# Performance work log

Measured on AMD Instinct MI355X. Metric: run time of the kernel, lower is better.

Reference implementation:

```python
import jax, jax.numpy as jnp
import numpy as np

B, S, D = 4, 2048, 1024
E, TOP_K = 8, 2
N_FF = 4096
H = int(2 * N_FF / 3)  # 2730, Expert hidden when ffn_multiplier is None


def setup_inputs() -> dict:
    key = jax.random.key(0)
    ks = jax.random.split(key, 8)
    s = 0.02
    return {
        "x": jax.random.normal(ks[0], (B, S, D), jnp.float32),
        "noise": jax.random.normal(ks[1], (B, S, E), jnp.float32),
        "w_route": jax.random.normal(ks[2], (D, E), jnp.float32) * s,
        "b_route": jnp.zeros((E,), jnp.float32),
        "w_noise": jax.random.normal(ks[3], (D, E), jnp.float32) * s,
        "b_noise": jnp.zeros((E,), jnp.float32),
        "w_proj": jax.random.normal(ks[4], (E, D, 2 * H), jnp.float32) * s,  # SwiGLU proj per expert
        "w_down": jax.random.normal(ks[5], (E, H, D), jnp.float32) * s,
    }


def reference(x, noise, w_route, b_route, w_noise, b_noise, w_proj, w_down):
    b, s, d = x.shape
    e = w_route.shape[1]
    n = b * s
    capacity = int(n * TOP_K / e * 1.0)  # capacity_factor = 1.0

    # --- NoisyTopkRouter (temperature = 1.0) ---
    logits = jnp.einsum("bsd,de->bse", x, w_route) + b_route
    noise_scale = jax.nn.softplus(jnp.einsum("bsd,de->bse", x, w_noise) + b_noise)
    noisy = logits + noise * noise_scale
    top_v, top_i = jax.lax.top_k(noisy, TOP_K)  # [b,s,k]
    # softmax over -inf-filled sparse logits == softmax over the top-k values,
    # scattered back to the expert axis
    probs_k = jax.nn.softmax(top_v, axis=-1)  # [b,s,k]
    routing = jnp.sum(jax.nn.one_hot(top_i, e, dtype=x.dtype) * probs_k[..., None], axis=-2)  # [b,s,e]
    router_prob = routing.mean(axis=(0, 1))
    aux_loss = jnp.sum((router_prob - 1.0 / e) ** 2)

    # --- dispatch ---
    flat_x = x.reshape(n, d)
    flat_gate = routing.reshape(n, e)
    hit = jnp.any(top_i.reshape(n, TOP_K)[:, :, None] == jnp.arange(e)[None, None, :], axis=1)  # [n,e]

    def per_expert(mask_e, gate_e, wp, wd):
        # keep first `capacity` selected tokens, in token order (matches torch nonzero order)
        keep = mask_e & (jnp.cumsum(mask_e) <= capacity)
        sel = jnp.argsort(~keep, stable=True)[:capacity]  # selected token ids first, in order
        valid = keep[sel].astype(flat_x.dtype)
        xin = flat_x[sel]  # [capacity, d]
        x1, x2 = jnp.split(xin @ wp, 2, axis=-1)
        out = (jax.nn.silu(x1) * x2) @ wd  # [capacity, d]
        w = gate_e[sel] * valid
        return sel, out * w[:, None]

    sel, contrib = jax.vmap(per_expert)(hit.T, flat_gate.T, w_proj, w_down)  # [e,cap], [e,cap,d]
    updates = jnp.zeros_like(flat_x).at[sel.reshape(-1)].add(contrib.reshape(-1, d))
    return updates.reshape(b, s, d), aux_loss
```

## Files before the change

kernel.cpp:

```cpp
#include <hip/hip_runtime.h>
#include <cstdint>
#include <cstddef>

#define NTOK 8192
#define DMODEL 1024
#define NEXP 8
#define CAP 2048
#define HFF 2730
#define HFF2 5460
#define KPAD 2752

typedef float f32x4 __attribute__((ext_vector_type(4)));
typedef __attribute__((ext_vector_type(8))) short short8;

__device__ inline unsigned short f2bf(float f) {
  union { float f; unsigned u; } v; v.f = f;
  unsigned u = v.u;
  return (unsigned short)((u + 0x7FFFu + ((u >> 16) & 1u)) >> 16);
}
__device__ inline float bf2f(unsigned short s) {
  union { unsigned u; float f; } v; v.u = ((unsigned)s) << 16; return v.f;
}

typedef __attribute__((address_space(1))) const void g_void;
typedef __attribute__((address_space(3))) void l_void;
__device__ __forceinline__ void dma16(const void* g, void* l) {
  __builtin_amdgcn_global_load_lds((g_void*)g, (l_void*)l, 16, 0, 0);
}

__global__ void cast_x_kernel(const float* __restrict__ x, unsigned short* __restrict__ xb) {
  size_t i = ((size_t)blockIdx.x * 256 + threadIdx.x) * 8;
  float4 v0 = *(const float4*)(x + i);
  float4 v1 = *(const float4*)(x + i + 4);
  union { short8 v; unsigned short s[8]; } p;
  p.s[0] = f2bf(v0.x); p.s[1] = f2bf(v0.y); p.s[2] = f2bf(v0.z); p.s[3] = f2bf(v0.w);
  p.s[4] = f2bf(v1.x); p.s[5] = f2bf(v1.y); p.s[6] = f2bf(v1.z); p.s[7] = f2bf(v1.w);
  *(short8*)(xb + i) = p.v;
}

__global__ void router_kernel(const float* __restrict__ x,
                              const float* __restrict__ noise,
                              const float* __restrict__ w_route,
                              const float* __restrict__ b_route,
                              const float* __restrict__ w_noise,
                              const float* __restrict__ b_noise,
                              int* __restrict__ topi,
                              float* __restrict__ gates) {
  const int lane = threadIdx.x & 63;
  const int wave = threadIdx.x >> 6;
  const int tok = blockIdx.x * 4 + wave;
  const float* xr = x + (size_t)tok * DMODEL;

  double aR[8], aN[8];
#pragma unroll
  for (int e = 0; e < 8; e++) { aR[e] = 0.0; aN[e] = 0.0; }

  for (int d = lane; d < DMODEL; d += 64) {
    double xv = (double)xr[d];
    const float* wr = w_route + d * 8;
    const float* wn = w_noise + d * 8;
#pragma unroll
    for (int e = 0; e < 8; e++) {
      aR[e] += xv * (double)wr[e];
      aN[e] += xv * (double)wn[e];
    }
  }
#pragma unroll
  for (int off = 32; off > 0; off >>= 1) {
#pragma unroll
    for (int e = 0; e < 8; e++) {
      aR[e] += __shfl_down(aR[e], (unsigned)off, 64);
      aN[e] += __shfl_down(aN[e], (unsigned)off, 64);
    }
  }
  if (lane == 0) {
    double nv[8];
#pragma unroll
    for (int e = 0; e < 8; e++) {
      double lg = aR[e] + (double)b_route[e];
      double ns = aN[e] + (double)b_noise[e];
      double sp = fmax(ns, 0.0) + log1p(exp(-fabs(ns)));
      nv[e] = lg + (double)noise[(size_t)tok * 8 + e] * sp;
    }
    int i0 = 0;
#pragma unroll
    for (int e = 1; e < 8; e++) if (nv[e] > nv[i0]) i0 = e;
    int i1 = (i0 == 0) ? 1 : 0;
#pragma unroll
    for (int e = 0; e < 8; e++) if (e != i0 && nv[e] > nv[i1]) i1 = e;
    double r = exp(nv[i1] - nv[i0]);
    float g0 = (float)(1.0 / (1.0 + r));
    float g1 = (float)(r / (1.0 + r));
    topi[tok * 2] = i0; topi[tok * 2 + 1] = i1;
    gates[tok * 2] = g0; gates[tok * 2 + 1] = g1;
  }
}

__global__ void aux_kernel(const int* __restrict__ topi,
                           const float* __restrict__ gates,
                           float* __restrict__ out) {
  const int t = threadIdx.x;
  float s[8];
#pragma unroll
  for (int e = 0; e < 8; e++) s[e] = 0.f;
  for (int i = t; i < NTOK; i += 256) {
    int i0 = topi[2 * i], i1 = topi[2 * i + 1];
    float g0 = gates[2 * i], g1 = gates[2 * i + 1];
#pragma unroll
    for (int e = 0; e < 8; e++)
      s[e] += (i0 == e ? g0 : 0.f) + (i1 == e ? g1 : 0.f);
  }
  __shared__ float sh[256][8];
#pragma unroll
  for (int e = 0; e < 8; e++) sh[t][e] = s[e];
  __syncthreads();
  for (int stride = 128; stride > 0; stride >>= 1) {
    if (t < stride) {
#pragma unroll
      for (int e = 0; e < 8; e++) sh[t][e] += sh[t + stride][e];
    }
    __syncthreads();
  }
  if (t == 0) {
    float aux = 0.f;
#pragma unroll
    for (int e = 0; e < 8; e++) {
      float p = sh[0][e] / (float)NTOK - 0.125f;
      aux += p * p;
    }
    out[(size_t)NTOK * DMODEL] = aux;
  }
}

__global__ void dispatch_kernel(const int* __restrict__ topi,
                                const float* __restrict__ gates,
                                int* __restrict__ sel,
                                float* __restrict__ gsel,
                                int* __restrict__ slot) {
  const int e = blockIdx.x;
  const int t = threadIdx.x;
  const int lane = t & 63;
  const int w = t >> 6;
  __shared__ int waveCnt[16];
  __shared__ int runningS;
  if (t == 0) runningS = 0;
  __syncthreads();

  for (int base = 0; base < NTOK; base += 1024) {
    int tok = base + t;
    int i0 = topi[2 * tok], i1 = topi[2 * tok + 1];
    bool hit = (i0 == e) || (i1 == e);
    int kth = (i0 == e) ? 0 : 1;
    float g = gates[2 * tok + kth];
    unsigned long long m = __ballot(hit);
    int prefix = __popcll(m & ((1ull << lane) - 1ull));
    if (lane == 63) waveCnt[w] = prefix + (hit ? 1 : 0);
    __syncthreads();
    int off = runningS;
    for (int ww = 0; ww < w; ww++) off += waveCnt[ww];
    int pos = off + prefix;
    if (hit) {
      if (pos < CAP) {
        sel[e * CAP + pos] = tok; gsel[e * CAP + pos] = g;
        slot[2 * tok + kth] = pos;
      } else {
        slot[2 * tok + kth] = -1;
      }
    }
    __syncthreads();
    if (t == 0) {
      int sacc = 0;
#pragma unroll
      for (int ww = 0; ww < 16; ww++) sacc += waveCnt[ww];
      runningS += sacc;
    }
    __syncthreads();
  }
  for (int p = runningS + t; p < CAP; p += 1024) { sel[e * CAP + p] = 0; gsel[e * CAP + p] = 0.f; }
}

__global__ void transpose_wp_kernel(const float* __restrict__ wp,
                                    unsigned short* __restrict__ wpT) {
  const int e = blockIdx.z, d0 = blockIdx.y * 32, f0 = blockIdx.x * 32;
  __shared__ unsigned short tile[32][33];
  const int t = threadIdx.x;
  {
    int ld = t >> 3, lf4 = (t & 7) * 4;
    if (f0 + lf4 < HFF2) {
      float4 v = *(const float4*)(wp + (size_t)e * DMODEL * HFF2 + (size_t)(d0 + ld) * HFF2 + f0 + lf4);
      tile[ld][lf4 + 0] = f2bf(v.x);
      tile[ld][lf4 + 1] = f2bf(v.y);
      tile[ld][lf4 + 2] = f2bf(v.z);
      tile[ld][lf4 + 3] = f2bf(v.w);
    }
  }
  __syncthreads();
  {
    int lf = t >> 3, ldq = (t & 7) * 4;
    if (f0 + lf < HFF2) {
      ushort4 o = make_ushort4(tile[ldq + 0][lf], tile[ldq + 1][lf],
                               tile[ldq + 2][lf], tile[ldq + 3][lf]);
      *(ushort4*)(wpT + (size_t)e * HFF2 * DMODEL + (size_t)(f0 + lf) * DMODEL + d0 + ldq) = o;
    }
  }
}

__global__ void transpose_wd_kernel(const float* __restrict__ wd,
                                    unsigned short* __restrict__ wdT) {
  const int e = blockIdx.z, d0 = blockIdx.y * 32, k0 = blockIdx.x * 32;
  __shared__ unsigned short tile[32][33];
  const int t = threadIdx.x;
  {
    int lk = t >> 3, ld4 = (t & 7) * 4;
    int k = k0 + lk;
    if (k < HFF) {
      float4 v = *(const float4*)(wd + (size_t)e * HFF * DMODEL + (size_t)k * DMODEL + d0 + ld4);
      tile[lk][ld4 + 0] = f2bf(v.x);
      tile[lk][ld4 + 1] = f2bf(v.y);
      tile[lk][ld4 + 2] = f2bf(v.z);
      tile[lk][ld4 + 3] = f2bf(v.w);
    } else {
      tile[lk][ld4 + 0] = 0; tile[lk][ld4 + 1] = 0;
      tile[lk][ld4 + 2] = 0; tile[lk][ld4 + 3] = 0;
    }
  }
  __syncthreads();
  {
    int ld = t >> 3, lkq = (t & 7) * 4;
    ushort4 o = make_ushort4(tile[lkq + 0][ld], tile[lkq + 1][ld],
                             tile[lkq + 2][ld], tile[lkq + 3][ld]);
    *(ushort4*)(wdT + (size_t)e * DMODEL * KPAD + (size_t)(d0 + ld) * KPAD + k0 + lkq) = o;
  }
}

__global__ __launch_bounds__(256, 2)
void gemm1_kernel(const unsigned short* __restrict__ xb,
                  const unsigned short* __restrict__ wpT,
                  const int* __restrict__ sel,
                  unsigned short* __restrict__ h) {
  const int e = blockIdx.z;
  const int m0 = blockIdx.x * 128;
  const int n0 = blockIdx.y * 128;

  __shared__ __align__(16) unsigned short As[2 * 4096];
  __shared__ __align__(16) unsigned short B1s[2 * 4096];
  __shared__ __align__(16) unsigned short B2s[2 * 4096];

  const int t = threadIdx.x;
  const int lane = t & 63;
  const int w = t >> 6;
  const int wm = (w >> 1) * 64;
  const int wn = (w & 1) * 64;
  const int fr = lane & 15;
  const int fq = lane >> 4;
  const int csw = (fq ^ ((fr >> 1) & 3)) * 8;

  const int r0 = t >> 2;
  const int sw = ((t & 3) ^ ((t >> 3) & 3)) * 8;
  const int tok0 = sel[e * CAP + m0 + r0];
  const int tok1 = sel[e * CAP + m0 + 64 + r0];
  const unsigned short* ga0 = xb + (size_t)tok0 * DMODEL + sw;
  const unsigned short* ga1 = xb + (size_t)tok1 * DMODEL + sw;
  const size_t ebase = (size_t)e * HFF2;
  int c0 = n0 + r0;       if (c0 >= HFF) c0 = HFF - 1;
  int c1 = n0 + 64 + r0;  if (c1 >= HFF) c1 = HFF - 1;
  const unsigned short* gb10 = wpT + (ebase + (size_t)c0) * DMODEL + sw;
  const unsigned short* gb11 = wpT + (ebase + (size_t)c1) * DMODEL + sw;
  const unsigned short* gb20 = wpT + (ebase + (size_t)(HFF + c0)) * DMODEL + sw;
  const unsigned short* gb21 = wpT + (ebase + (size_t)(HFF + c1)) * DMODEL + sw;

  const int dOff = (w * 16) * 32;

  f32x4 acc1[4][4], acc2[4][4];
#pragma unroll
  for (int i = 0; i < 4; i++)
#pragma unroll
    for (int j = 0; j < 4; j++) { acc1[i][j] = (f32x4)0.f; acc2[i][j] = (f32x4)0.f; }

  auto stage = [&](int k0, int buf) {
    const int bo = buf * 4096;
    dma16(ga0 + k0, As + bo + dOff);
    dma16(ga1 + k0, As + bo + 2048 + dOff);
    dma16(gb10 + k0, B1s + bo + dOff);
    dma16(gb11 + k0, B1s + bo + 2048 + dOff);
    dma16(gb20 + k0, B2s + bo + dOff);
    dma16(gb21 + k0, B2s + bo + 2048 + dOff);
  };

  stage(0, 0);
  for (int k0 = 0; k0 < DMODEL; k0 += 32) {
    const int cur = (k0 >> 5) & 1;
    __syncthreads();
    if (k0 + 32 < DMODEL) stage(k0 + 32, cur ^ 1);

    const unsigned short* Ab = As + cur * 4096;
    const unsigned short* B1b = B1s + cur * 4096;
    const unsigned short* B2b = B2s + cur * 4096;
    short8 a[4], b1[4], b2[4];
#pragma unroll
    for (int i = 0; i < 4; i++)
      a[i] = *(const short8*)(Ab + (wm + i * 16 + fr) * 32 + csw);
#pragma unroll
    for (int j = 0; j < 4; j++) {
      b1[j] = *(const short8*)(B1b + (wn + j * 16 + fr) * 32 + csw);
      b2[j] = *(const short8*)(B2b + (wn + j * 16 + fr) * 32 + csw);
    }
#pragma unroll
    for (int i = 0; i < 4; i++)
#pragma unroll
      for (int j = 0; j < 4; j++) {
        acc1[i][j] = __builtin_amdgcn_mfma_f32_16x16x32_bf16(a[i], b1[j], acc1[i][j], 0, 0, 0);
        acc2[i][j] = __builtin_amdgcn_mfma_f32_16x16x32_bf16(a[i], b2[j], acc2[i][j], 0, 0, 0);
      }
  }

#pragma unroll
  for (int i = 0; i < 4; i++) {
#pragma unroll
    for (int j = 0; j < 4; j++) {
      const int col = n0 + wn + j * 16 + fr;
      if (col < KPAD) {
#pragma unroll
        for (int r = 0; r < 4; r++) {
          const int row = m0 + wm + i * 16 + fq * 4 + r;
          float v1 = acc1[i][j][r], v2 = acc2[i][j][r];
          float hv = (col < HFF) ? (v1 / (1.f + __expf(-v1))) * v2 : 0.f;
          h[((size_t)e * CAP + row) * KPAD + col] = f2bf(hv);
        }
      }
    }
  }
}

__global__ __launch_bounds__(256, 3)
void gemm2_kernel(const unsigned short* __restrict__ h,
                  const unsigned short* __restrict__ wdT,
                  unsigned short* __restrict__ contrib) {
  const int e = blockIdx.z;
  const int m0 = blockIdx.x * 128;
  const int n0 = blockIdx.y * 128;

  __shared__ __align__(16) unsigned short As[2 * 4096];
  __shared__ __align__(16) unsigned short Bs[2 * 4096];

  const int t = threadIdx.x;
  const int lane = t & 63;
  const int w = t >> 6;
  const int wm = (w >> 1) * 64;
  const int wn = (w & 1) * 64;
  const int fr = lane & 15;
  const int fq = lane >> 4;
  const int csw = (fq ^ ((fr >> 1) & 3)) * 8;

  const int r0 = t >> 2;
  const int sw = ((t & 3) ^ ((t >> 3) & 3)) * 8;
  const unsigned short* ga0 = h + ((size_t)e * CAP + m0 + r0) * KPAD + sw;
  const unsigned short* ga1 = h + ((size_t)e * CAP + m0 + 64 + r0) * KPAD + sw;
  const unsigned short* gb0 = wdT + ((size_t)e * DMODEL + n0 + r0) * KPAD + sw;
  const unsigned short* gb1 = wdT + ((size_t)e * DMODEL + n0 + 64 + r0) * KPAD + sw;

  const int dOff = (w * 16) * 32;

  f32x4 acc[4][4];
#pragma unroll
  for (int i = 0; i < 4; i++)
#pragma unroll
    for (int j = 0; j < 4; j++) acc[i][j] = (f32x4)0.f;

  auto stage = [&](int k0, int buf) {
    const int bo = buf * 4096;
    dma16(ga0 + k0, As + bo + dOff);
    dma16(ga1 + k0, As + bo + 2048 + dOff);
    dma16(gb0 + k0, Bs + bo + dOff);
    dma16(gb1 + k0, Bs + bo + 2048 + dOff);
  };

  stage(0, 0);
  for (int k0 = 0; k0 < KPAD; k0 += 32) {
    const int cur = (k0 >> 5) & 1;
    __syncthreads();
    if (k0 + 32 < KPAD) stage(k0 + 32, cur ^ 1);

    const unsigned short* Ab = As + cur * 4096;
    const unsigned short* Bb = Bs + cur * 4096;
    short8 a[4], b[4];
#pragma unroll
    for (int i = 0; i < 4; i++)
      a[i] = *(const short8*)(Ab + (wm + i * 16 + fr) * 32 + csw);
#pragma unroll
    for (int j = 0; j < 4; j++)
      b[j] = *(const short8*)(Bb + (wn + j * 16 + fr) * 32 + csw);
#pragma unroll
    for (int i = 0; i < 4; i++)
#pragma unroll
      for (int j = 0; j < 4; j++)
        acc[i][j] = __builtin_amdgcn_mfma_f32_16x16x32_bf16(a[i], b[j], acc[i][j], 0, 0, 0);
  }

#pragma unroll
  for (int i = 0; i < 4; i++) {
#pragma unroll
    for (int j = 0; j < 4; j++) {
      const int col = n0 + wn + j * 16 + fr;
#pragma unroll
      for (int r = 0; r < 4; r++) {
        const int row = m0 + wm + i * 16 + fq * 4 + r;
        contrib[((size_t)e * CAP + row) * DMODEL + col] = f2bf(acc[i][j][r]);
      }
    }
  }
}

__global__ void combine_kernel(const unsigned short* __restrict__ contrib,
                               const int* __restrict__ topi,
                               const int* __restrict__ slot,
                               const float* __restrict__ gates,
                               float* __restrict__ out) {
  const int tok = blockIdx.x;
  const int t = threadIdx.x;
  const int e0 = topi[2 * tok], e1 = topi[2 * tok + 1];
  const int s0 = slot[2 * tok], s1 = slot[2 * tok + 1];
  const float g0 = gates[2 * tok], g1 = gates[2 * tok + 1];
  float4 acc = make_float4(0.f, 0.f, 0.f, 0.f);
  if (s0 >= 0) {
    ushort4 c = *(const ushort4*)(contrib + ((size_t)(e0 * CAP + s0)) * DMODEL + t * 4);
    acc.x += g0 * bf2f(c.x); acc.y += g0 * bf2f(c.y);
    acc.z += g0 * bf2f(c.z); acc.w += g0 * bf2f(c.w);
  }
  if (s1 >= 0) {
    ushort4 c = *(const ushort4*)(contrib + ((size_t)(e1 * CAP + s1)) * DMODEL + t * 4);
    acc.x += g1 * bf2f(c.x); acc.y += g1 * bf2f(c.y);
    acc.z += g1 * bf2f(c.z); acc.w += g1 * bf2f(c.w);
  }
  *(float4*)(out + (size_t)tok * DMODEL + t * 4) = acc;
}

extern "C" void kernel_launch(void* const* d_in, const int* in_sizes, int n_in,
                              void* d_out, int out_size, void* d_ws, size_t ws_size,
                              hipStream_t stream) {
  const float* x = (const float*)d_in[0];
  const float* noise = (const float*)d_in[1];
  const float* w_route = (const float*)d_in[2];
  const float* b_route = (const float*)d_in[3];
  const float* w_noise = (const float*)d_in[4];
  const float* b_noise = (const float*)d_in[5];
  const float* w_proj = (const float*)d_in[6];
  const float* w_down = (const float*)d_in[7];
  float* out = (float*)d_out;

  char* ws = (char*)d_ws;
  const size_t WT_BYTES = (size_t)NEXP * HFF2 * DMODEL * 2;
  const size_t WDT_BYTES = (size_t)NEXP * DMODEL * KPAD * 2;
  const size_t H_BYTES = (size_t)NEXP * CAP * KPAD * 2;
  unsigned short* wT = (unsigned short*)ws;
  unsigned short* contrib = (unsigned short*)(ws + WDT_BYTES);
  unsigned short* hbuf = (unsigned short*)(ws + WT_BYTES);
  char* p = ws + WT_BYTES + H_BYTES;
  int* sel = (int*)p;          p += (size_t)NEXP * CAP * 4;
  float* gsel = (float*)p;     p += (size_t)NEXP * CAP * 4;
  int* topi = (int*)p;         p += (size_t)NTOK * 2 * 4;
  float* gates = (float*)p;    p += (size_t)NTOK * 2 * 4;
  int* slot = (int*)p;

  unsigned short* xb = (unsigned short*)d_out;

  hipLaunchKernelGGL(cast_x_kernel, dim3(NTOK * DMODEL / (256 * 8)), dim3(256), 0, stream, x, xb);
  hipLaunchKernelGGL(router_kernel, dim3(NTOK / 4), dim3(256), 0, stream,
                     x, noise, w_route, b_route, w_noise, b_noise, topi, gates);
  hipLaunchKernelGGL(dispatch_kernel, dim3(NEXP), dim3(1024), 0, stream, topi, gates, sel, gsel, slot);
  hipLaunchKernelGGL(transpose_wp_kernel, dim3(171, 32, NEXP), dim3(256), 0, stream, w_proj, wT);
  hipLaunchKernelGGL(gemm1_kernel, dim3(16, 22, NEXP), dim3(256), 0, stream, xb, wT, sel, hbuf);
  hipLaunchKernelGGL(transpose_wd_kernel, dim3(KPAD / 32, DMODEL / 32, NEXP), dim3(256), 0, stream, w_down, wT);
  hipLaunchKernelGGL(gemm2_kernel, dim3(16, DMODEL / 128, NEXP), dim3(256), 0, stream,
                     hbuf, wT, contrib);
  hipLaunchKernelGGL(combine_kernel, dim3(NTOK), dim3(256), 0, stream,
                     contrib, topi, slot, gates, out);
  hipLaunchKernelGGL(aux_kernel, dim3(1), dim3(256), 0, stream, topi, gates, out);
}
```

Before: 862.6 us.

## Enlarge GEMM tiles to 512 threads with 4-stage async LDS pipeline

Both expert GEMMs move to 512-thread blocks with larger tiles (256x128 for gemm1, 256x256 for gemm2). A 4-buffer shared-memory ring fed three stages ahead replaces the double buffer, with explicit vmcnt waits and raw barriers in place of __syncthreads. Loads are interleaved with MFMA groups and wave priority is raised around the MFMAs. The aim is better data reuse per block and hiding global latency, at the cost of higher register and LDS pressure and fewer blocks in the grid.

```diff
diff --git a/kernel.cpp b/kernel.cpp
--- a/kernel.cpp
+++ b/kernel.cpp
@@ -233,24 +233,22 @@
   }
 }
 
-__global__ __launch_bounds__(256, 2)
+__global__ __launch_bounds__(512, 2)
 void gemm1_kernel(const unsigned short* __restrict__ xb,
                   const unsigned short* __restrict__ wpT,
                   const int* __restrict__ sel,
                   unsigned short* __restrict__ h) {
   const int e = blockIdx.z;
-  const int m0 = blockIdx.x * 128;
+  const int m0 = blockIdx.x * 256;
   const int n0 = blockIdx.y * 128;
 
-  __shared__ __align__(16) unsigned short As[2 * 4096];
-  __shared__ __align__(16) unsigned short B1s[2 * 4096];
-  __shared__ __align__(16) unsigned short B2s[2 * 4096];
+  __shared__ __align__(16) unsigned short smem[4 * 16384];
 
   const int t = threadIdx.x;
   const int lane = t & 63;
   const int w = t >> 6;
-  const int wm = (w >> 1) * 64;
-  const int wn = (w & 1) * 64;
+  const int wr = w >> 2;
+  const int wc = w & 3;
   const int fr = lane & 15;
   const int fq = lane >> 4;
   const int csw = (fq ^ ((fr >> 1) & 3)) * 8;
@@ -258,71 +256,85 @@
   const int r0 = t >> 2;
   const int sw = ((t & 3) ^ ((t >> 3) & 3)) * 8;
   const int tok0 = sel[e * CAP + m0 + r0];
-  const int tok1 = sel[e * CAP + m0 + 64 + r0];
+  const int tok1 = sel[e * CAP + m0 + 128 + r0];
   const unsigned short* ga0 = xb + (size_t)tok0 * DMODEL + sw;
   const unsigned short* ga1 = xb + (size_t)tok1 * DMODEL + sw;
   const size_t ebase = (size_t)e * HFF2;
-  int c0 = n0 + r0;       if (c0 >= HFF) c0 = HFF - 1;
-  int c1 = n0 + 64 + r0;  if (c1 >= HFF) c1 = HFF - 1;
-  const unsigned short* gb10 = wpT + (ebase + (size_t)c0) * DMODEL + sw;
-  const unsigned short* gb11 = wpT + (ebase + (size_t)c1) * DMODEL + sw;
-  const unsigned short* gb20 = wpT + (ebase + (size_t)(HFF + c0)) * DMODEL + sw;
-  const unsigned short* gb21 = wpT + (ebase + (size_t)(HFF + c1)) * DMODEL + sw;
-
-  const int dOff = (w * 16) * 32;
-
-  f32x4 acc1[4][4], acc2[4][4];
-#pragma unroll
-  for (int i = 0; i < 4; i++)
-#pragma unroll
-    for (int j = 0; j < 4; j++) { acc1[i][j] = (f32x4)0.f; acc2[i][j] = (f32x4)0.f; }
-
-  auto stage = [&](int k0, int buf) {
-    const int bo = buf * 4096;
-    dma16(ga0 + k0, As + bo + dOff);
-    dma16(ga1 + k0, As + bo + 2048 + dOff);
-    dma16(gb10 + k0, B1s + bo + dOff);
-    dma16(gb11 + k0, B1s + bo + 2048 + dOff);
-    dma16(gb20 + k0, B2s + bo + dOff);
-    dma16(gb21 + k0, B2s + bo + 2048 + dOff);
+  int c0 = n0 + r0; if (c0 >= HFF) c0 = HFF - 1;
+  const unsigned short* gb1 = wpT + (ebase + (size_t)c0) * DMODEL + sw;
+  const unsigned short* gb2 = wpT + (ebase + (size_t)(HFF + c0)) * DMODEL + sw;
+
+  const int dOff = w * 1024;
+
+  f32x4 acc1[8][2], acc2[8][2];
+#pragma unroll
+  for (int i = 0; i < 8; i++)
+#pragma unroll
+    for (int j = 0; j < 2; j++) { acc1[i][j] = (f32x4)0.f; acc2[i][j] = (f32x4)0.f; }
+
+  auto stageA = [&](int kt) {
+    char* b = (char*)smem + (size_t)(kt & 3) * 32768;
+    const int k0 = kt * 32;
+    dma16(ga0 + k0, b + dOff);
+    dma16(ga1 + k0, b + 8192 + dOff);
   };
-
-  stage(0, 0);
-  for (int k0 = 0; k0 < DMODEL; k0 += 32) {
-    const int cur = (k0 >> 5) & 1;
-    __syncthreads();
-    if (k0 + 32 < DMODEL) stage(k0 + 32, cur ^ 1);
-
-    const unsigned short* Ab = As + cur * 4096;
-    const unsigned short* B1b = B1s + cur * 4096;
-    const unsigned short* B2b = B2s + cur * 4096;
-    short8 a[4], b1[4], b2[4];
-#pragma unroll
-    for (int i = 0; i < 4; i++)
-      a[i] = *(const short8*)(Ab + (wm + i * 16 + fr) * 32 + csw);
-#pragma unroll
-    for (int j = 0; j < 4; j++) {
-      b1[j] = *(const short8*)(B1b + (wn + j * 16 + fr) * 32 + csw);
-      b2[j] = *(const short8*)(B2b + (wn + j * 16 + fr) * 32 + csw);
-    }
-#pragma unroll
-    for (int i = 0; i < 4; i++)
-#pragma unroll
-      for (int j = 0; j < 4; j++) {
+  auto stageB = [&](int kt) {
+    char* b = (char*)smem + (size_t)(kt & 3) * 32768;
+    const int k0 = kt * 32;
+    dma16(gb1 + k0, b + 16384 + dOff);
+    dma16(gb2 + k0, b + 24576 + dOff);
+  };
+
+  stageA(0); stageB(0); stageA(1); stageB(1); stageA(2); stageB(2);
+
+  for (int kt = 0; kt < 32; ++kt) {
+    if (kt < 30)       asm volatile("s_waitcnt vmcnt(8)" ::: "memory");
+    else if (kt == 30) asm volatile("s_waitcnt vmcnt(4)" ::: "memory");
+    else               asm volatile("s_waitcnt vmcnt(0)" ::: "memory");
+    __builtin_amdgcn_s_barrier();
+    asm volatile("" ::: "memory");
+
+    const unsigned short* Ab  = smem + (kt & 3) * 16384;
+    const unsigned short* B1b = Ab + 8192;
+    const unsigned short* B2b = Ab + 12288;
+
+    short8 a[8], b1[2], b2[2];
+#pragma unroll
+    for (int i = 0; i < 8; i++)
+      a[i] = *(const short8*)(Ab + (wr * 128 + i * 16 + fr) * 32 + csw);
+#pragma unroll
+    for (int j = 0; j < 2; j++)
+      b1[j] = *(const short8*)(B1b + (wc * 32 + j * 16 + fr) * 32 + csw);
+    if (kt < 29) stageA(kt + 3);
+    __builtin_amdgcn_s_setprio(1);
+#pragma unroll
+    for (int i = 0; i < 8; i++)
+#pragma unroll
+      for (int j = 0; j < 2; j++)
         acc1[i][j] = __builtin_amdgcn_mfma_f32_16x16x32_bf16(a[i], b1[j], acc1[i][j], 0, 0, 0);
+    __builtin_amdgcn_s_setprio(0);
+#pragma unroll
+    for (int j = 0; j < 2; j++)
+      b2[j] = *(const short8*)(B2b + (wc * 32 + j * 16 + fr) * 32 + csw);
+    if (kt < 29) stageB(kt + 3);
+    __builtin_amdgcn_s_setprio(1);
+#pragma unroll
+    for (int i = 0; i < 8; i++)
+#pragma unroll
+      for (int j = 0; j < 2; j++)
         acc2[i][j] = __builtin_amdgcn_mfma_f32_16x16x32_bf16(a[i], b2[j], acc2[i][j], 0, 0, 0);
-      }
-  }
-
-#pragma unroll
-  for (int i = 0; i < 4; i++) {
-#pragma unroll
-    for (int j = 0; j < 4; j++) {
-      const int col = n0 + wn + j * 16 + fr;
+    __builtin_amdgcn_s_setprio(0);
+  }
+
+#pragma unroll
+  for (int i = 0; i < 8; i++) {
+#pragma unroll
+    for (int j = 0; j < 2; j++) {
+      const int col = n0 + wc * 32 + j * 16 + fr;
       if (col < KPAD) {
 #pragma unroll
         for (int r = 0; r < 4; r++) {
-          const int row = m0 + wm + i * 16 + fq * 4 + r;
+          const int row = m0 + wr * 128 + i * 16 + fq * 4 + r;
           float v1 = acc1[i][j][r], v2 = acc2[i][j][r];
           float hv = (col < HFF) ? (v1 / (1.f + __expf(-v1))) * v2 : 0.f;
           h[((size_t)e * CAP + row) * KPAD + col] = f2bf(hv);
@@ -332,22 +344,21 @@
   }
 }
 
-__global__ __launch_bounds__(256, 3)
+__global__ __launch_bounds__(512, 2)
 void gemm2_kernel(const unsigned short* __restrict__ h,
                   const unsigned short* __restrict__ wdT,
                   unsigned short* __restrict__ contrib) {
   const int e = blockIdx.z;
-  const int m0 = blockIdx.x * 128;
-  const int n0 = blockIdx.y * 128;
-
-  __shared__ __align__(16) unsigned short As[2 * 4096];
-  __shared__ __align__(16) unsigned short Bs[2 * 4096];
+  const int m0 = blockIdx.x * 256;
+  const int n0 = blockIdx.y * 256;
+
+  __shared__ __align__(16) unsigned short smem[4 * 16384];
 
   const int t = threadIdx.x;
   const int lane = t & 63;
   const int w = t >> 6;
-  const int wm = (w >> 1) * 64;
-  const int wn = (w & 1) * 64;
+  const int wr = w >> 2;
+  const int wc = w & 3;
   const int fr = lane & 15;
   const int fq = lane >> 4;
   const int csw = (fq ^ ((fr >> 1) & 3)) * 8;
@@ -355,56 +366,68 @@
   const int r0 = t >> 2;
   const int sw = ((t & 3) ^ ((t >> 3) & 3)) * 8;
   const unsigned short* ga0 = h + ((size_t)e * CAP + m0 + r0) * KPAD + sw;
-  const unsigned short* ga1 = h + ((size_t)e * CAP + m0 + 64 + r0) * KPAD + sw;
+  const unsigned short* ga1 = h + ((size_t)e * CAP + m0 + 128 + r0) * KPAD + sw;
   const unsigned short* gb0 = wdT + ((size_t)e * DMODEL + n0 + r0) * KPAD + sw;
-  const unsigned short* gb1 = wdT + ((size_t)e * DMODEL + n0 + 64 + r0) * KPAD + sw;
-
-  const int dOff = (w * 16) * 32;
-
-  f32x4 acc[4][4];
-#pragma unroll
-  for (int i = 0; i < 4; i++)
+  const unsigned short* gb1 = wdT + ((size_t)e * DMODEL + n0 + 128 + r0) * KPAD + sw;
+
+  const int dOff = w * 1024;
+
+  f32x4 acc[8][4];
+#pragma unroll
+  for (int i = 0; i < 8; i++)
 #pragma unroll
     for (int j = 0; j < 4; j++) acc[i][j] = (f32x4)0.f;
 
-  auto stage = [&](int k0, int buf) {
-    const int bo = buf * 4096;
-    dma16(ga0 + k0, As + bo + dOff);
-    dma16(ga1 + k0, As + bo + 2048 + dOff);
-    dma16(gb0 + k0, Bs + bo + dOff);
-    dma16(gb1 + k0, Bs + bo + 2048 + dOff);
+  auto stageA = [&](int kt) {
+    char* b = (char*)smem + (size_t)(kt & 3) * 32768;
+    const int k0 = kt * 32;
+    dma16(ga0 + k0, b + dOff);
+    dma16(ga1 + k0, b + 8192 + dOff);
   };
-
-  stage(0, 0);
-  for (int k0 = 0; k0 < KPAD; k0 += 32) {
-    const int cur = (k0 >> 5) & 1;
-    __syncthreads();
-    if (k0 + 32 < KPAD) stage(k0 + 32, cur ^ 1);
-
-    const unsigned short* Ab = As + cur * 4096;
-    const unsigned short* Bb = Bs + cur * 4096;
-    short8 a[4], b[4];
-#pragma unroll
-    for (int i = 0; i < 4; i++)
-      a[i] = *(const short8*)(Ab + (wm + i * 16 + fr) * 32 + csw);
+  auto stageB = [&](int kt) {
+    char* b = (char*)smem + (size_t)(kt & 3) * 32768;
+    const int k0 = kt * 32;
+    dma16(gb0 + k0, b + 16384 + dOff);
+    dma16(gb1 + k0, b + 24576 + dOff);
+  };
+
+  stageA(0); stageB(0); stageA(1); stageB(1); stageA(2); stageB(2);
+
+  for (int kt = 0; kt < 86; ++kt) {
+    if (kt < 84)       asm volatile("s_waitcnt vmcnt(8)" ::: "memory");
+    else if (kt == 84) asm volatile("s_waitcnt vmcnt(4)" ::: "memory");
+    else               asm volatile("s_waitcnt vmcnt(0)" ::: "memory");
+    __builtin_amdgcn_s_barrier();
+    asm volatile("" ::: "memory");
+
+    const unsigned short* Ab = smem + (kt & 3) * 16384;
+    const unsigned short* Bb = Ab + 8192;
+
+    short8 a[8], b[4];
+#pragma unroll
+    for (int i = 0; i < 8; i++)
+      a[i] = *(const short8*)(Ab + (wr * 128 + i * 16 + fr) * 32 + csw);
 #pragma unroll
     for (int j = 0; j < 4; j++)
-      b[j] = *(const short8*)(Bb + (wn + j * 16 + fr) * 32 + csw);
-#pragma unroll
-    for (int i = 0; i < 4; i++)
+      b[j] = *(const short8*)(Bb + (wc * 64 + j * 16 + fr) * 32 + csw);
+    if (kt < 83) { stageA(kt + 3); stageB(kt + 3); }
+    __builtin_amdgcn_s_setprio(1);
+#pragma unroll
+    for (int i = 0; i < 8; i++)
 #pragma unroll
       for (int j = 0; j < 4; j++)
         acc[i][j] = __builtin_amdgcn_mfma_f32_16x16x32_bf16(a[i], b[j], acc[i][j], 0, 0, 0);
-  }
-
-#pragma unroll
-  for (int i = 0; i < 4; i++) {
+    __builtin_amdgcn_s_setprio(0);
+  }
+
+#pragma unroll
+  for (int i = 0; i < 8; i++) {
 #pragma unroll
     for (int j = 0; j < 4; j++) {
-      const int col = n0 + wn + j * 16 + fr;
+      const int col = n0 + wc * 64 + j * 16 + fr;
 #pragma unroll
       for (int r = 0; r < 4; r++) {
-        const int row = m0 + wm + i * 16 + fq * 4 + r;
+        const int row = m0 + wr * 128 + i * 16 + fq * 4 + r;
         contrib[((size_t)e * CAP + row) * DMODEL + col] = f2bf(acc[i][j][r]);
       }
     }
@@ -469,9 +492,9 @@
                      x, noise, w_route, b_route, w_noise, b_noise, topi, gates);
   hipLaunchKernelGGL(dispatch_kernel, dim3(NEXP), dim3(1024), 0, stream, topi, gates, sel, gsel, slot);
   hipLaunchKernelGGL(transpose_wp_kernel, dim3(171, 32, NEXP), dim3(256), 0, stream, w_proj, wT);
-  hipLaunchKernelGGL(gemm1_kernel, dim3(16, 22, NEXP), dim3(256), 0, stream, xb, wT, sel, hbuf);
+  hipLaunchKernelGGL(gemm1_kernel, dim3(CAP / 256, 22, NEXP), dim3(512), 0, stream, xb, wT, sel, hbuf);
   hipLaunchKernelGGL(transpose_wd_kernel, dim3(KPAD / 32, DMODEL / 32, NEXP), dim3(256), 0, stream, w_down, wT);
-  hipLaunchKernelGGL(gemm2_kernel, dim3(16, DMODEL / 128, NEXP), dim3(256), 0, stream,
+  hipLaunchKernelGGL(gemm2_kernel, dim3(CAP / 256, DMODEL / 256, NEXP), dim3(512), 0, stream,
                      hbuf, wT, contrib);
   hipLaunchKernelGGL(combine_kernel, dim3(NTOK), dim3(256), 0, stream,
                      contrib, topi, slot, gates, out);
```

New measurement: 791.5 us. 8.2% less time.
